# Kernel tuning notes

Measured on AMD Instinct MI355X. Metric: run time of the kernel, lower is better.

Reference implementation:

```python
import jax, jax.numpy as jnp
import numpy as np

ITER_ROUTING = 3
FINAL_LAMBDA = 0.01
EPS = 1e-9

N = 4
CHILD_SPACE = 12
KERNEL = 3
STRIDE = 1
CHILD_CAPS = 16
PARENT_CAPS = 32
POSE = 16


def _routing_map(child_space, k, s):
    # (child_space^2, parent_space^2) binary map: child c feeds parent p.
    parent_space = (child_space - k) // s + 1
    m = np.zeros((child_space * child_space, parent_space * parent_space), np.float32)
    for pr in range(parent_space):
        for pc in range(parent_space):
            p = pr * parent_space + pc
            for r in range(k):
                for c in range(k):
                    m[(pr * s + r) * child_space + (pc * s + c), p] = 1.0
    return m


def setup_inputs() -> dict:
    key = jax.random.key(0)
    k1, k2, k3, k4 = jax.random.split(key, 4)
    parent_space = (CHILD_SPACE - KERNEL) // STRIDE + 1
    kk = KERNEL * KERNEL
    votes = jax.random.normal(k1, (N * parent_space * parent_space, kk * CHILD_CAPS, PARENT_CAPS, POSE), jnp.float32)
    acts = jax.random.uniform(k2, (N * parent_space * parent_space, kk * CHILD_CAPS, 1), dtype=jnp.float32)
    beta_v = jax.random.normal(k3, (1, 1, 1, 1, PARENT_CAPS, 1), jnp.float32)
    beta_a = jax.random.normal(k4, (1, 1, 1, 1, PARENT_CAPS, 1), jnp.float32)
    srm = jnp.asarray(_routing_map(CHILD_SPACE, KERNEL, STRIDE))
    return {"votes_ij": votes, "activations_i": acts, "beta_v": beta_v, "beta_a": beta_a,
            "spatial_routing_matrix": srm, "batch_size": N, "kk": kk}


def _em_routing(votes_ij, activations_i, beta_v, beta_a, srm, batch_size, kk):
    Nb = batch_size
    C2, P2 = srm.shape  # child_space^2, parent_space^2
    P = int(round(P2 ** 0.5))
    K_total, O, ch = votes_ij.shape[1], votes_ij.shape[2], votes_ij.shape[3]
    child_caps = K_total // kk

    votes = votes_ij.reshape(Nb, P, P, K_total, O, ch)
    act_i = activations_i.reshape(Nb, P, P, K_total, 1, 1)

    # children per parent, ascending child index (stable argsort on -1/0 values)
    cidx = jnp.argsort(-srm, axis=0)[:kk].T           # (P2, kk)
    seg = cidx.reshape(-1)                            # (P2*kk,) child id per (parent, slot)
    ppc = jnp.sum(srm, axis=1)                        # parents-per-child, (C2,)
    # init_rr: 1 / (parents_per_child * parent_caps + 1e-9), gathered per parent slot
    rr0 = (1.0 / (ppc[cidx] * O + 1e-9)).reshape(1, P, P, kk, 1, 1)
    rr = jnp.broadcast_to(rr0, (1, P, P, kk, child_caps, O)).reshape(1, P, P, K_total, O, 1)

    layer_norm_factor = 100.0 / (float(K_total) / float(O))

    def m_step(rr, it):
        lam = FINAL_LAMBDA * (1.0 - 0.95 ** (it + 1))
        rr_prime = rr * act_i                                            # (N,P,P,K,O,1)
        rr_prime_sum = jnp.sum(rr_prime, axis=-3, keepdims=True)         # (N,P,P,1,O,1)
        mean_j = jnp.sum(rr_prime * votes, axis=-3, keepdims=True) / (rr_prime_sum + EPS)
        var_j = jnp.sum(rr_prime * jnp.square(votes - mean_j), axis=-3, keepdims=True) / (rr_prime_sum + EPS)
        cost_j_h = (beta_v + 0.5 * jnp.log(var_j + EPS)) * rr_prime_sum * layer_norm_factor
        cost_j = jnp.sum(cost_j_h, axis=-1, keepdims=True)               # (N,P,P,1,O,1)
        cost_mean = jnp.mean(cost_j, axis=-2, keepdims=True)
        cost_stdv = jnp.sqrt(jnp.sum(jnp.square(cost_j - cost_mean), axis=-2, keepdims=True) / O)
        act_j = jax.nn.sigmoid(lam * (beta_a + (cost_mean - cost_j) / (cost_stdv + EPS)))
        return act_j, mean_j, var_j

    def e_step(act_j, mean_j, var_j):
        # log N(vote; mean_j, var_j) per parent + log activation
        o_p0 = -jnp.sum(jnp.square(votes - mean_j) / (2.0 * var_j), axis=-1, keepdims=True)
        o_p2 = -0.5 * jnp.sum(jnp.log(2.0 * np.pi * var_j), axis=-1, keepdims=True)
        zz = jnp.log(act_j + EPS) + o_p0 + o_p2                          # (N,P,P,K,O,1)
        # softmax over ALL parents of each child (spatial kk slots x parent_caps),
        # done via segment reductions keyed by child id (== sparse/softmax/dense of original)
        z = jnp.moveaxis(zz.reshape(Nb, P2 * kk, child_caps, O), 1, 0)   # (P2*kk, N, cc, O)
        m = jax.ops.segment_max(jnp.max(z, axis=-1), seg, num_segments=C2)  # (C2, N, cc)
        m = jnp.where(jnp.isinf(m), 0.0, m)
        e = jnp.exp(z - m[seg][..., None])
        denom = jax.ops.segment_sum(jnp.sum(e, axis=-1), seg, num_segments=C2)
        rr_new = e / denom[seg][..., None]
        return jnp.moveaxis(rr_new, 0, 1).reshape(Nb, P, P, K_total, O, 1)

    for it in range(ITER_ROUTING):
        act_j, mean_j, var_j = m_step(rr, it)
        if it < ITER_ROUTING - 1:
            rr = e_step(act_j, mean_j, var_j)

    poses_j = mean_j[:, :, :, 0]        # (N,P,P,O,16)
    activations_j = act_j[:, :, :, 0]   # (N,P,P,O,1)
    return poses_j, activations_j


def reference(votes_ij, activations_i, beta_v, beta_a, spatial_routing_matrix, batch_size, kk):
    return _em_routing(votes_ij, activations_i, beta_v, beta_a, spatial_routing_matrix, batch_size, kk)
```

## Files before the change

### kernel.cpp

```cpp
#include <hip/hip_runtime.h>
#include <hip/hip_fp16.h>
#include <math.h>

#define NB     4
#define P      10
#define P2     100
#define CS     12
#define CCAPS  16
#define KTOT   144
#define O      32
#define POSE   16
#define VSZ    73728
#define EPSF   1e-9f
#define LNF    22.2222222222222222f
#define TWO_PI 6.28318530717958647f
#define NBP    400
#define NKQ    3
#define KPU    48
#define SUNITS (NBP*NKQ)
#define NCQ    2
#define CZG    (NB*CS*CS*NCQ)

#define LAM0 0.0005f
#define LAM1 0.000975f
#define LAM2 0.00142625f

__device__ float g_m1 [SUNITS*512];
__device__ float g_m2 [SUNITS*512];
__device__ float g_sv [SUNITS*O];
__device__ float g_pm [NBP*9*NCQ*1024];
__device__ float g_ps [NBP*9*NCQ*32];
__device__ float g_mean[NBP*512];
__device__ float g_i2v [NBP*512];
__device__ float g_zpre[NBP*O];

__device__ __forceinline__ int npar(int x) {
    int a = x + 1, b = CS - x;
    int m = a < 3 ? a : 3;
    return m < b ? m : b;
}

__device__ __forceinline__ void up8(uint4 u, float* f) {
    float2 a = __half22float2(*(__half2*)&u.x);
    float2 b = __half22float2(*(__half2*)&u.y);
    float2 c = __half22float2(*(__half2*)&u.z);
    float2 d = __half22float2(*(__half2*)&u.w);
    f[0] = a.x; f[1] = a.y; f[2] = b.x; f[3] = b.y;
    f[4] = c.x; f[5] = c.y; f[6] = d.x; f[7] = d.y;
}

__global__ __launch_bounds__(256)
void v_kernel(const float* __restrict__ votes, const float* __restrict__ acts,
              __half* __restrict__ hv)
{
    __shared__ float actl[KPU];
    __shared__ __align__(16) float rrp[KPU*O];
    __shared__ float4 lm1[256];
    __shared__ float4 lm2[256];
    __shared__ float  lss[256];

    const int tid = threadIdx.x;
    const int u   = blockIdx.x;
    const int bp  = u / NKQ;
    const int kq  = u - bp * NKQ;
    const int k0  = kq * KPU;
    const int ks  = tid >> 7;
    const int q   = tid & 127;
    const int o   = q >> 2;

    if (tid < KPU) actl[tid] = acts[bp * KTOT + k0 + tid];
    __syncthreads();

    for (int f = tid; f < KPU * O / 4; f += 256) {
        int kl = f >> 3;
        int kg = k0 + kl, kslot = kg >> 4;
        int kr = kslot / 3, kc = kslot - kr * 3;
        int p = bp % P2, pr = p / P, pc = p - pr * P;
        float ppc = (float)(npar(pr + kr) * npar(pc + kc));
        float r = actl[kl] / (ppc * 32.0f + EPSF);
        ((float4*)rrp)[f] = make_float4(r, r, r, r);
    }
    __syncthreads();

    const float* vb  = votes + (size_t)bp * VSZ + (size_t)(k0 + ks * 24) * 512 + q * 4;
    __half*      hb  = hv    + (size_t)bp * VSZ + (size_t)(k0 + ks * 24) * 512 + q * 4;
    const float* rr0 = rrp + (ks * 24) * O + o;
    float  s  = 0.f;
    float4 m1 = make_float4(0.f, 0.f, 0.f, 0.f);
    float4 m2 = make_float4(0.f, 0.f, 0.f, 0.f);
    #pragma unroll 8
    for (int i = 0; i < 24; ++i) {
        float  rp = rr0[i * O];
        float4 v  = *(const float4*)(vb + i * 512);
        s += rp;
        m1.x += rp * v.x;       m1.y += rp * v.y;
        m1.z += rp * v.z;       m1.w += rp * v.w;
        m2.x += rp * v.x * v.x; m2.y += rp * v.y * v.y;
        m2.z += rp * v.z * v.z; m2.w += rp * v.w * v.w;
        __half2 ha  = __floats2half2_rn(v.x, v.y);
        __half2 hbv = __floats2half2_rn(v.z, v.w);
        uint2 st;
        st.x = *(unsigned int*)&ha;
        st.y = *(unsigned int*)&hbv;
        *(uint2*)(hb + i * 512) = st;
    }
    lm1[tid] = m1; lm2[tid] = m2; lss[tid] = s;
    __syncthreads();

    if (tid < 128) {
        float4 a = lm1[tid], b = lm1[tid + 128];
        m1 = make_float4(a.x + b.x, a.y + b.y, a.z + b.z, a.w + b.w);
        a = lm2[tid]; b = lm2[tid + 128];
        m2 = make_float4(a.x + b.x, a.y + b.y, a.z + b.z, a.w + b.w);
        s = lss[tid] + lss[tid + 128];
        ((float4*)g_m1)[u * 128 + tid] = m1;
        ((float4*)g_m2)[u * 128 + tid] = m2;
        if ((tid & 3) == 0) g_sv[u * O + (tid >> 2)] = s;
    }
}

__global__ __launch_bounds__(128)
void f0_kernel(const float* __restrict__ beta_v,
               const float* __restrict__ beta_a, float lam)
{
    __shared__ float costl[O];
    const int tid = threadIdx.x;
    const int o = tid >> 2, c4 = tid & 3;
    const int bp = blockIdx.x;

    float4 m1 = make_float4(0.f, 0.f, 0.f, 0.f);
    float4 m2 = make_float4(0.f, 0.f, 0.f, 0.f);
    float  s  = 0.f;
    #pragma unroll
    for (int j = 0; j < NKQ; ++j) {
        float4 a = ((const float4*)g_m1)[(bp * NKQ + j) * 128 + tid];
        float4 b = ((const float4*)g_m2)[(bp * NKQ + j) * 128 + tid];
        m1.x += a.x; m1.y += a.y; m1.z += a.z; m1.w += a.w;
        m2.x += b.x; m2.y += b.y; m2.z += b.z; m2.w += b.w;
        s += g_sv[(bp * NKQ + j) * O + o];
    }
    float denom = s + EPSF;
    float4 mean = make_float4(m1.x/denom, m1.y/denom, m1.z/denom, m1.w/denom);
    float4 var;
    var.x = fmaxf(m2.x/denom - mean.x*mean.x, 1e-30f);
    var.y = fmaxf(m2.y/denom - mean.y*mean.y, 1e-30f);
    var.z = fmaxf(m2.z/denom - mean.z*mean.z, 1e-30f);
    var.w = fmaxf(m2.w/denom - mean.w*mean.w, 1e-30f);
    float4 i2 = make_float4(0.5f/var.x, 0.5f/var.y, 0.5f/var.z, 0.5f/var.w);
    float lve = logf(var.x+EPSF)+logf(var.y+EPSF)+logf(var.z+EPSF)+logf(var.w+EPSF);
    float lv2 = logf(TWO_PI*var.x)+logf(TWO_PI*var.y)+logf(TWO_PI*var.z)+logf(TWO_PI*var.w);
    lve += __shfl_xor(lve,1); lve += __shfl_xor(lve,2);
    lv2 += __shfl_xor(lv2,1); lv2 += __shfl_xor(lv2,2);
    if (c4 == 0) costl[o] = (16.f*beta_v[o] + 0.5f*lve) * s * LNF;
    __syncthreads();
    float cm = 0.f;
    #pragma unroll
    for (int i = 0; i < O; ++i) cm += costl[i];
    cm *= (1.f/32.f);
    float sq = 0.f;
    #pragma unroll
    for (int i = 0; i < O; ++i) { float d = costl[i]-cm; sq += d*d; }
    float cstd = sqrtf(sq * (1.f/32.f));
    float aj = 1.f/(1.f+expf(-lam*(beta_a[o] + (cm-costl[o])/(cstd+EPSF))));
    ((float4*)g_mean)[bp*128+tid] = mean;
    ((float4*)g_i2v)[bp*128+tid]  = i2;
    if (c4 == 0) g_zpre[bp*O+o] = logf(aj+EPSF) - 0.5f*lv2;
}

__global__ __launch_bounds__(256)
void cz_kernel(const __half* __restrict__ hv, const float* __restrict__ acts)
{
    __shared__ float red[4*32*33];

    const int tid = threadIdx.x;
    const int ccl = tid >> 5;
    const int o   = tid & 31;
    const int blk = blockIdx.x;
    const int ccq = blk & (NCQ-1);
    const int bc  = blk / NCQ;
    const int b   = bc / (CS*CS);
    const int c   = bc - b*(CS*CS);
    const int cr  = c / CS, cl = c - cr*CS;
    const int cc  = ccq*8 + ccl;

    int   bpps[9];
    float ez[9];
    float av[9];
    float vmax = -1e30f;

    #pragma unroll
    for (int kr = 0; kr < 3; ++kr) {
        #pragma unroll
        for (int kc = 0; kc < 3; ++kc) {
            const int si  = kr*3 + kc;
            const int pr_ = cr - kr, pc_ = cl - kc;
            const bool ok = (pr_ >= 0 && pr_ < P && pc_ >= 0 && pc_ < P);
            int bpp = ok ? (b*P2 + pr_*P + pc_) : -1;
            bpps[si] = bpp;
            float z = -1e30f;
            if (ok) {
                const __half* vb = hv + (size_t)bpp*VSZ + (size_t)(si*16+cc)*512 + o*16;
                uint4 u0 = *(const uint4*)(vb);
                uint4 u1 = *(const uint4*)(vb + 8);
                float f[16]; up8(u0, f); up8(u1, f + 8);
                const float4* mm = (const float4*)(g_mean + (size_t)bpp*512 + o*16);
                const float4* iv = (const float4*)(g_i2v  + (size_t)bpp*512 + o*16);
                float t = 0.f;
                #pragma unroll
                for (int j4 = 0; j4 < 4; ++j4) {
                    float4 m = mm[j4], w = iv[j4];
                    float d0 = f[j4*4  ]-m.x, d1 = f[j4*4+1]-m.y;
                    float d2 = f[j4*4+2]-m.z, d3 = f[j4*4+3]-m.w;
                    t += d0*d0*w.x + d1*d1*w.y + d2*d2*w.z + d3*d3*w.w;
                }
                z = g_zpre[bpp*O + o] - t;
                av[si] = acts[bpp*KTOT + si*16 + cc];
            }
            ez[si] = z;
            vmax = fmaxf(vmax, z);
        }
    }
    vmax = fmaxf(vmax, __shfl_xor(vmax, 1));
    vmax = fmaxf(vmax, __shfl_xor(vmax, 2));
    vmax = fmaxf(vmax, __shfl_xor(vmax, 4));
    vmax = fmaxf(vmax, __shfl_xor(vmax, 8));
    vmax = fmaxf(vmax, __shfl_xor(vmax, 16));
    float ps = 0.f;
    #pragma unroll
    for (int si = 0; si < 9; ++si) {
        float e = (ez[si] > -1e29f) ? expf(ez[si] - vmax) : 0.f;
        ez[si] = e;
        ps += e;
    }
    ps += __shfl_xor(ps, 1);
    ps += __shfl_xor(ps, 2);
    ps += __shfl_xor(ps, 4);
    ps += __shfl_xor(ps, 8);
    ps += __shfl_xor(ps, 16);
    const float inv = 1.f / ps;

    #pragma unroll
    for (int si = 0; si < 9; ++si) {
        const int bpp = bpps[si];
        if (bpp >= 0) {
            float rp = ez[si] * inv * av[si];
            const __half* vb = hv + (size_t)bpp*VSZ + (size_t)(si*16+cc)*512 + o*16;
            uint4 u0 = *(const uint4*)(vb);
            uint4 u1 = *(const uint4*)(vb + 8);
            float f[16]; up8(u0, f); up8(u1, f + 8);
            float m1[16], m2[16];
            #pragma unroll
            for (int j = 0; j < 16; ++j) { m1[j] = rp*f[j]; m2[j] = rp*f[j]*f[j]; }
            float s = rp;
            #pragma unroll
            for (int j = 0; j < 16; ++j) {
                m1[j] += __shfl_xor(m1[j], 32);
                m2[j] += __shfl_xor(m2[j], 32);
            }
            s += __shfl_xor(s, 32);
            if ((ccl & 1) == 0) {
                float* r = red + ((ccl >> 1)*32 + o)*33;
                #pragma unroll
                for (int j = 0; j < 16; ++j) { r[j] = m1[j]; r[16+j] = m2[j]; }
                r[32] = s;
            }
            __syncthreads();
            if (tid < 32) {
                float* dst = g_pm + ((size_t)(bpp*9 + si)*NCQ + ccq)*1024;
                float sa = 0.f;
                #pragma unroll
                for (int j4 = 0; j4 < 8; ++j4) {
                    float4 acc = make_float4(0.f, 0.f, 0.f, 0.f);
                    #pragma unroll
                    for (int w = 0; w < 4; ++w) {
                        const float* r = red + (w*32 + tid)*33 + j4*4;
                        acc.x += r[0]; acc.y += r[1]; acc.z += r[2]; acc.w += r[3];
                    }
                    int half = j4 >> 2, j4l = j4 & 3;
                    ((float4*)(dst + half*512))[tid*4 + j4l] = acc;
                }
                #pragma unroll
                for (int w = 0; w < 4; ++w) sa += red[(w*32 + tid)*33 + 32];
                g_ps[((bpp*9 + si)*NCQ + ccq)*32 + tid] = sa;
            }
            __syncthreads();
        }
    }
}

template<bool LAST>
__global__ __launch_bounds__(128)
void f12_kernel(const float* __restrict__ beta_v,
                const float* __restrict__ beta_a,
                float* __restrict__ out, float lam)
{
    __shared__ float costl[O];
    const int tid = threadIdx.x;
    const int o = tid >> 2, c4 = tid & 3;
    const int bp = blockIdx.x;

    float4 m1 = make_float4(0.f, 0.f, 0.f, 0.f);
    float4 m2 = make_float4(0.f, 0.f, 0.f, 0.f);
    float  s  = 0.f;
    #pragma unroll
    for (int si = 0; si < 9; ++si) {
        #pragma unroll
        for (int qq = 0; qq < NCQ; ++qq) {
            const float* base = g_pm + ((size_t)(bp*9 + si)*NCQ + qq)*1024;
            float4 a = ((const float4*)base)[tid];
            float4 b = ((const float4*)(base + 512))[tid];
            m1.x += a.x; m1.y += a.y; m1.z += a.z; m1.w += a.w;
            m2.x += b.x; m2.y += b.y; m2.z += b.z; m2.w += b.w;
            s += g_ps[((bp*9 + si)*NCQ + qq)*32 + o];
        }
    }
    float denom = s + EPSF;
    float4 mean = make_float4(m1.x/denom, m1.y/denom, m1.z/denom, m1.w/denom);
    float4 var;
    var.x = fmaxf(m2.x/denom - mean.x*mean.x, 1e-30f);
    var.y = fmaxf(m2.y/denom - mean.y*mean.y, 1e-30f);
    var.z = fmaxf(m2.z/denom - mean.z*mean.z, 1e-30f);
    var.w = fmaxf(m2.w/denom - mean.w*mean.w, 1e-30f);
    float4 i2 = make_float4(0.5f/var.x, 0.5f/var.y, 0.5f/var.z, 0.5f/var.w);
    float lve = logf(var.x+EPSF)+logf(var.y+EPSF)+logf(var.z+EPSF)+logf(var.w+EPSF);
    float lv2 = logf(TWO_PI*var.x)+logf(TWO_PI*var.y)+logf(TWO_PI*var.z)+logf(TWO_PI*var.w);
    lve += __shfl_xor(lve,1); lve += __shfl_xor(lve,2);
    lv2 += __shfl_xor(lv2,1); lv2 += __shfl_xor(lv2,2);
    if (c4 == 0) costl[o] = (16.f*beta_v[o] + 0.5f*lve) * s * LNF;
    __syncthreads();
    float cm = 0.f;
    #pragma unroll
    for (int i = 0; i < O; ++i) cm += costl[i];
    cm *= (1.f/32.f);
    float sq = 0.f;
    #pragma unroll
    for (int i = 0; i < O; ++i) { float d = costl[i]-cm; sq += d*d; }
    float cstd = sqrtf(sq * (1.f/32.f));
    float aj = 1.f/(1.f+expf(-lam*(beta_a[o] + (cm-costl[o])/(cstd+EPSF))));

    if (LAST) {
        ((float4*)out)[bp*128 + tid] = mean;
        if (c4 == 0) out[(size_t)NBP*512 + bp*O + o] = aj;
    } else {
        ((float4*)g_mean)[bp*128 + tid] = mean;
        ((float4*)g_i2v)[bp*128 + tid]  = i2;
        if (c4 == 0) g_zpre[bp*O + o] = logf(aj+EPSF) - 0.5f*lv2;
    }
}

extern "C" void kernel_launch(void* const* d_in, const int* in_sizes, int n_in,
                              void* d_out, int out_size, void* d_ws, size_t ws_size,
                              hipStream_t stream)
{
    (void)in_sizes; (void)n_in; (void)out_size; (void)ws_size;

    const float* votes = (const float*)d_in[0];
    const float* acts  = (const float*)d_in[1];
    const float* bv    = (const float*)d_in[2];
    const float* ba    = (const float*)d_in[3];
    float* out = (float*)d_out;
    __half* hv = (__half*)d_ws;

    v_kernel<<<dim3(SUNITS), dim3(256), 0, stream>>>(votes, acts, hv);
    f0_kernel<<<dim3(NBP), dim3(128), 0, stream>>>(bv, ba, LAM0);
    cz_kernel<<<dim3(CZG), dim3(256), 0, stream>>>(hv, acts);
    f12_kernel<false><<<dim3(NBP), dim3(128), 0, stream>>>(bv, ba, out, LAM1);
    cz_kernel<<<dim3(CZG), dim3(256), 0, stream>>>(hv, acts);
    f12_kernel<true ><<<dim3(NBP), dim3(128), 0, stream>>>(bv, ba, out, LAM2);
}
```

Before: 304.7 us.

## Split E-step scatter into separate rr write and parent-major statistics kernel

The child-major cz kernel no longer reduces weighted vote moments per parent slot with block-wide syncs inside a 9-iteration loop. It now only writes routing coefficients times activations to a global buffer. A new parent-major s16 kernel then reads the fp16 votes and these coefficients and accumulates partial first and second moments, and the f kernel reduces them unchanged. This removes the repeated __syncthreads and shared-memory reduction from cz, at the cost of an extra kernel launch per iteration, a second pass over the fp16 votes, and an extra global rr buffer.

After: 271.8 us. -10.8%, faster.

```diff
diff --git a/kernel.cpp b/kernel.cpp
--- a/kernel.cpp
+++ b/kernel.cpp
@@ -28,8 +28,7 @@
 __device__ float g_m1 [SUNITS*512];
 __device__ float g_m2 [SUNITS*512];
 __device__ float g_sv [SUNITS*O];
-__device__ float g_pm [NBP*9*NCQ*1024];
-__device__ float g_ps [NBP*9*NCQ*32];
+__device__ float g_rrp[NBP*KTOT*O];
 __device__ float g_mean[NBP*512];
 __device__ float g_i2v [NBP*512];
 __device__ float g_zpre[NBP*O];
@@ -119,9 +118,76 @@
     }
 }
 
+__global__ __launch_bounds__(256)
+void s16_kernel(const __half* __restrict__ hv)
+{
+    __shared__ __align__(16) float rrp[KPU*O];
+    __shared__ float4 lm1[512];
+    __shared__ float4 lm2[512];
+    __shared__ float  lss[256];
+
+    const int tid = threadIdx.x;
+    const int u   = blockIdx.x;
+    const int bp  = u / NKQ;
+    const int kq  = u - bp * NKQ;
+    const int k0  = kq * KPU;
+    const int ks  = tid >> 6;
+    const int qp  = tid & 63;
+    const int o   = qp >> 1;
+
+    for (int f = tid; f < KPU * O / 4; f += 256)
+        ((float4*)rrp)[f] = ((const float4*)(g_rrp + (size_t)bp * (KTOT * O) + k0 * O))[f];
+    __syncthreads();
+
+    const __half* vb = hv + (size_t)bp * VSZ + (size_t)(k0 + ks * 12) * 512 + qp * 8;
+    const float* rr0 = rrp + (ks * 12) * O + o;
+    float s = 0.f;
+    float m1[8], m2[8];
+    #pragma unroll
+    for (int j = 0; j < 8; ++j) { m1[j] = 0.f; m2[j] = 0.f; }
+    #pragma unroll 4
+    for (int i = 0; i < 12; ++i) {
+        float rp = rr0[i * O];
+        uint4 u4 = *(const uint4*)(vb + i * 512);
+        float f[8]; up8(u4, f);
+        s += rp;
+        #pragma unroll
+        for (int j = 0; j < 8; ++j) {
+            m1[j] += rp * f[j];
+            m2[j] += rp * f[j] * f[j];
+        }
+    }
+    lm1[tid*2]   = make_float4(m1[0], m1[1], m1[2], m1[3]);
+    lm1[tid*2+1] = make_float4(m1[4], m1[5], m1[6], m1[7]);
+    lm2[tid*2]   = make_float4(m2[0], m2[1], m2[2], m2[3]);
+    lm2[tid*2+1] = make_float4(m2[4], m2[5], m2[6], m2[7]);
+    lss[tid] = s;
+    __syncthreads();
+
+    if (tid < 64) {
+        #pragma unroll
+        for (int j = 0; j < 2; ++j) {
+            float4 a0 = lm1[(tid)*2+j],       a1 = lm1[(64+tid)*2+j];
+            float4 a2 = lm1[(128+tid)*2+j],   a3 = lm1[(192+tid)*2+j];
+            float4 r = make_float4(a0.x+a1.x+a2.x+a3.x, a0.y+a1.y+a2.y+a3.y,
+                                   a0.z+a1.z+a2.z+a3.z, a0.w+a1.w+a2.w+a3.w);
+            ((float4*)g_m1)[u * 128 + tid*2 + j] = r;
+            float4 b0 = lm2[(tid)*2+j],       b1 = lm2[(64+tid)*2+j];
+            float4 b2 = lm2[(128+tid)*2+j],   b3 = lm2[(192+tid)*2+j];
+            float4 r2 = make_float4(b0.x+b1.x+b2.x+b3.x, b0.y+b1.y+b2.y+b3.y,
+                                    b0.z+b1.z+b2.z+b3.z, b0.w+b1.w+b2.w+b3.w);
+            ((float4*)g_m2)[u * 128 + tid*2 + j] = r2;
+        }
+        float sr = lss[tid] + lss[64+tid] + lss[128+tid] + lss[192+tid];
+        if ((tid & 1) == 0) g_sv[u * O + (tid >> 1)] = sr;
+    }
+}
+
+template<bool LAST>
 __global__ __launch_bounds__(128)
-void f0_kernel(const float* __restrict__ beta_v,
-               const float* __restrict__ beta_a, float lam)
+void f_kernel(const float* __restrict__ beta_v,
+              const float* __restrict__ beta_a,
+              float* __restrict__ out, float lam)
 {
     __shared__ float costl[O];
     const int tid = threadIdx.x;
@@ -162,16 +228,20 @@
     for (int i = 0; i < O; ++i) { float d = costl[i]-cm; sq += d*d; }
     float cstd = sqrtf(sq * (1.f/32.f));
     float aj = 1.f/(1.f+expf(-lam*(beta_a[o] + (cm-costl[o])/(cstd+EPSF))));
-    ((float4*)g_mean)[bp*128+tid] = mean;
-    ((float4*)g_i2v)[bp*128+tid]  = i2;
-    if (c4 == 0) g_zpre[bp*O+o] = logf(aj+EPSF) - 0.5f*lv2;
+
+    if (LAST) {
+        ((float4*)out)[bp*128 + tid] = mean;
+        if (c4 == 0) out[(size_t)NBP*512 + bp*O + o] = aj;
+    } else {
+        ((float4*)g_mean)[bp*128 + tid] = mean;
+        ((float4*)g_i2v)[bp*128 + tid]  = i2;
+        if (c4 == 0) g_zpre[bp*O + o] = logf(aj+EPSF) - 0.5f*lv2;
+    }
 }
 
 __global__ __launch_bounds__(256)
 void cz_kernel(const __half* __restrict__ hv, const float* __restrict__ acts)
 {
-    __shared__ float red[4*32*33];
-
     const int tid = threadIdx.x;
     const int ccl = tid >> 5;
     const int o   = tid & 31;
@@ -198,6 +268,7 @@
             int bpp = ok ? (b*P2 + pr_*P + pc_) : -1;
             bpps[si] = bpp;
             float z = -1e30f;
+            av[si] = 0.f;
             if (ok) {
                 const __half* vb = hv + (size_t)bpp*VSZ + (size_t)(si*16+cc)*512 + o*16;
                 uint4 u0 = *(const uint4*)(vb);
@@ -242,109 +313,8 @@
     #pragma unroll
     for (int si = 0; si < 9; ++si) {
         const int bpp = bpps[si];
-        if (bpp >= 0) {
-            float rp = ez[si] * inv * av[si];
-            const __half* vb = hv + (size_t)bpp*VSZ + (size_t)(si*16+cc)*512 + o*16;
-            uint4 u0 = *(const uint4*)(vb);
-            uint4 u1 = *(const uint4*)(vb + 8);
-            float f[16]; up8(u0, f); up8(u1, f + 8);
-            float m1[16], m2[16];
-            #pragma unroll
-            for (int j = 0; j < 16; ++j) { m1[j] = rp*f[j]; m2[j] = rp*f[j]*f[j]; }
-            float s = rp;
-            #pragma unroll
-            for (int j = 0; j < 16; ++j) {
-                m1[j] += __shfl_xor(m1[j], 32);
-                m2[j] += __shfl_xor(m2[j], 32);
-            }
-            s += __shfl_xor(s, 32);
-            if ((ccl & 1) == 0) {
-                float* r = red + ((ccl >> 1)*32 + o)*33;
-                #pragma unroll
-                for (int j = 0; j < 16; ++j) { r[j] = m1[j]; r[16+j] = m2[j]; }
-                r[32] = s;
-            }
-            __syncthreads();
-            if (tid < 32) {
-                float* dst = g_pm + ((size_t)(bpp*9 + si)*NCQ + ccq)*1024;
-                float sa = 0.f;
-                #pragma unroll
-                for (int j4 = 0; j4 < 8; ++j4) {
-                    float4 acc = make_float4(0.f, 0.f, 0.f, 0.f);
-                    #pragma unroll
-                    for (int w = 0; w < 4; ++w) {
-                        const float* r = red + (w*32 + tid)*33 + j4*4;
-                        acc.x += r[0]; acc.y += r[1]; acc.z += r[2]; acc.w += r[3];
-                    }
-                    int half = j4 >> 2, j4l = j4 & 3;
-                    ((float4*)(dst + half*512))[tid*4 + j4l] = acc;
-                }
-                #pragma unroll
-                for (int w = 0; w < 4; ++w) sa += red[(w*32 + tid)*33 + 32];
-                g_ps[((bpp*9 + si)*NCQ + ccq)*32 + tid] = sa;
-            }
-            __syncthreads();
-        }
-    }
-}
-
-template<bool LAST>
-__global__ __launch_bounds__(128)
-void f12_kernel(const float* __restrict__ beta_v,
-                const float* __restrict__ beta_a,
-                float* __restrict__ out, float lam)
-{
-    __shared__ float costl[O];
-    const int tid = threadIdx.x;
-    const int o = tid >> 2, c4 = tid & 3;
-    const int bp = blockIdx.x;
-
-    float4 m1 = make_float4(0.f, 0.f, 0.f, 0.f);
-    float4 m2 = make_float4(0.f, 0.f, 0.f, 0.f);
-    float  s  = 0.f;
-    #pragma unroll
-    for (int si = 0; si < 9; ++si) {
-        #pragma unroll
-        for (int qq = 0; qq < NCQ; ++qq) {
-            const float* base = g_pm + ((size_t)(bp*9 + si)*NCQ + qq)*1024;
-            float4 a = ((const float4*)base)[tid];
-            float4 b = ((const float4*)(base + 512))[tid];
-            m1.x += a.x; m1.y += a.y; m1.z += a.z; m1.w += a.w;
-            m2.x += b.x; m2.y += b.y; m2.z += b.z; m2.w += b.w;
-            s += g_ps[((bp*9 + si)*NCQ + qq)*32 + o];
-        }
-    }
-    float denom = s + EPSF;
-    float4 mean = make_float4(m1.x/denom, m1.y/denom, m1.z/denom, m1.w/denom);
-    float4 var;
-    var.x = fmaxf(m2.x/denom - mean.x*mean.x, 1e-30f);
-    var.y = fmaxf(m2.y/denom - mean.y*mean.y, 1e-30f);
-    var.z = fmaxf(m2.z/denom - mean.z*mean.z, 1e-30f);
-    var.w = fmaxf(m2.w/denom - mean.w*mean.w, 1e-30f);
-    float4 i2 = make_float4(0.5f/var.x, 0.5f/var.y, 0.5f/var.z, 0.5f/var.w);
-    float lve = logf(var.x+EPSF)+logf(var.y+EPSF)+logf(var.z+EPSF)+logf(var.w+EPSF);
-    float lv2 = logf(TWO_PI*var.x)+logf(TWO_PI*var.y)+logf(TWO_PI*var.z)+logf(TWO_PI*var.w);
-    lve += __shfl_xor(lve,1); lve += __shfl_xor(lve,2);
-    lv2 += __shfl_xor(lv2,1); lv2 += __shfl_xor(lv2,2);
-    if (c4 == 0) costl[o] = (16.f*beta_v[o] + 0.5f*lve) * s * LNF;
-    __syncthreads();
-    float cm = 0.f;
-    #pragma unroll
-    for (int i = 0; i < O; ++i) cm += costl[i];
-    cm *= (1.f/32.f);
-    float sq = 0.f;
-    #pragma unroll
-    for (int i = 0; i < O; ++i) { float d = costl[i]-cm; sq += d*d; }
-    float cstd = sqrtf(sq * (1.f/32.f));
-    float aj = 1.f/(1.f+expf(-lam*(beta_a[o] + (cm-costl[o])/(cstd+EPSF))));
-
-    if (LAST) {
-        ((float4*)out)[bp*128 + tid] = mean;
-        if (c4 == 0) out[(size_t)NBP*512 + bp*O + o] = aj;
-    } else {
-        ((float4*)g_mean)[bp*128 + tid] = mean;
-        ((float4*)g_i2v)[bp*128 + tid]  = i2;
-        if (c4 == 0) g_zpre[bp*O + o] = logf(aj+EPSF) - 0.5f*lv2;
+        if (bpp >= 0)
+            g_rrp[((size_t)bpp*KTOT + si*16 + cc)*32 + o] = ez[si] * inv * av[si];
     }
 }
 
@@ -362,9 +332,11 @@
     __half* hv = (__half*)d_ws;
 
     v_kernel<<<dim3(SUNITS), dim3(256), 0, stream>>>(votes, acts, hv);
-    f0_kernel<<<dim3(NBP), dim3(128), 0, stream>>>(bv, ba, LAM0);
+    f_kernel<false><<<dim3(NBP), dim3(128), 0, stream>>>(bv, ba, out, LAM0);
     cz_kernel<<<dim3(CZG), dim3(256), 0, stream>>>(hv, acts);
-    f12_kernel<false><<<dim3(NBP), dim3(128), 0, stream>>>(bv, ba, out, LAM1);
+    s16_kernel<<<dim3(SUNITS), dim3(256), 0, stream>>>(hv);
+    f_kernel<false><<<dim3(NBP), dim3(128), 0, stream>>>(bv, ba, out, LAM1);
     cz_kernel<<<dim3(CZG), dim3(256), 0, stream>>>(hv, acts);
-    f12_kernel<true ><<<dim3(NBP), dim3(128), 0, stream>>>(bv, ba, out, LAM2);
-}
+    s16_kernel<<<dim3(SUNITS), dim3(256), 0, stream>>>(hv);
+    f_kernel<true ><<<dim3(NBP), dim3(128), 0, stream>>>(bv, ba, out, LAM2);
+}
```
